# Optimization experiments

Measured on AMD Instinct MI355X. Metric: run time of the kernel, lower is better.

## Reference

```python
import jax, jax.numpy as jnp
import numpy as np

B, N, N_IN, N_OUT, NUM_ACTS = 65536, 512, 64, 16, 5


def setup_inputs() -> dict:
    key = jax.random.key(0)
    k1, k2, k3, k4 = jax.random.split(key, 4)
    input_values = jax.random.normal(k1, (B, N_IN), dtype=jnp.float32)
    # small weights so recurrent pre-activations stay in a sane range
    weight_matrix = jax.random.normal(k2, (N, N), dtype=jnp.float32) * 0.1
    biases = jax.random.normal(k3, (N,), dtype=jnp.float32) * 0.1
    act_ids = jax.random.randint(k4, (N,), 0, NUM_ACTS, dtype=jnp.int32)
    return {
        "input_values": input_values,
        "weight_matrix": weight_matrix,
        "biases": biases,
        "act_ids": act_ids,
    }


def _apply_lut_activations(total, act_ids):
    # Vectorized replacement for the per-neuron Python dispatch loop.
    # act_ids: [N] int, total: [B, N] float. Elementwise select fuses cleanly.
    conds = [act_ids[None, :] == k for k in range(NUM_ACTS)]
    branches = [
        jnp.tanh(total),                      # 0: tanh
        jax.nn.sigmoid(total),                # 1: sigmoid
        jax.nn.relu(total),                   # 2: relu
        jnp.where(total > 0, total, 0.01 * total),  # 3: leaky_relu
        total,                                # 4: identity
    ]
    return jnp.select(conds, branches, total)


def reference(input_values, weight_matrix, biases, act_ids):
    b, n_in = input_values.shape
    n = weight_matrix.shape[0]
    # forward_batch: states start at zeros (refractory multiply on zeros is a no-op),
    # input neurons (first N_IN indices) get the raw input values.
    states = jnp.zeros((b, n), dtype=input_values.dtype).at[:, :n_in].set(input_values)
    total_input = states @ weight_matrix + biases  # [B, N]
    activated = _apply_lut_activations(total_input, act_ids)
    # input-layer neurons keep their raw input values (loop skips layer == 'input')
    is_input = jnp.arange(n) < n_in  # [N]
    new_states = jnp.where(is_input[None, :], states, activated)
    # output neurons are the last N_OUT indices
    return new_states[:, n - N_OUT:]
```

## Files before the change

### kernel.cpp

```cpp
#include <hip/hip_runtime.h>
#include <math.h>


typedef __bf16 bf16x8 __attribute__((ext_vector_type(8)));
typedef float floatx4 __attribute__((ext_vector_type(4)));

#define NN_N 512
#define NN_NIN 64
#define NN_NOUT 16

__global__ __launch_bounds__(256) void NeuralNetwork_74466142978489_kernel(
    const float* __restrict__ x,
    const float* __restrict__ W,
    const float* __restrict__ bias,
    const int*   __restrict__ acts,
    float* __restrict__ out,
    int num_tiles)
{
    const int lane = threadIdx.x & 63;
    const int wave = (int)((blockIdx.x * blockDim.x + threadIdx.x) >> 6);
    const int nwaves = (int)((gridDim.x * blockDim.x) >> 6);
    const int m    = lane & 15;
    const int quad = lane >> 4;
    const int col  = m;
    const int gcol = NN_N - NN_NOUT + col;

    bf16x8 bfrag0, bfrag1;
#pragma unroll
    for (int j = 0; j < 8; ++j) {
        int k0 = quad * 8 + j;
        bfrag0[j] = (__bf16)W[(size_t)k0 * NN_N + gcol];
        bfrag1[j] = (__bf16)W[(size_t)(k0 + 32) * NN_N + gcol];
    }
    const float bval = bias[gcol];
    const int aid = acts[gcol];

    for (int tile = wave; tile < num_tiles; tile += nwaves) {
        const float* row = x + (size_t)(tile * 16 + m) * NN_NIN;

        floatx4 acc = {bval, bval, bval, bval};
#pragma unroll
        for (int t = 0; t < 2; ++t) {
            const float4 a0 = *(const float4*)(row + t * 32 + quad * 8);
            const float4 a1 = *(const float4*)(row + t * 32 + quad * 8 + 4);
            bf16x8 afrag;
            afrag[0] = (__bf16)a0.x; afrag[1] = (__bf16)a0.y;
            afrag[2] = (__bf16)a0.z; afrag[3] = (__bf16)a0.w;
            afrag[4] = (__bf16)a1.x; afrag[5] = (__bf16)a1.y;
            afrag[6] = (__bf16)a1.z; afrag[7] = (__bf16)a1.w;
            acc = __builtin_amdgcn_mfma_f32_16x16x32_bf16(
                afrag, (t == 0) ? bfrag0 : bfrag1, acc, 0, 0, 0);
        }

#pragma unroll
        for (int r = 0; r < 4; ++r) {
            float v = acc[r];
            float y;
            if (aid == 0) {
                y = 1.0f - 2.0f / (__expf(2.0f * v) + 1.0f);
            } else if (aid == 1) {
                y = 1.0f / (1.0f + __expf(-v));
            } else if (aid == 2) {
                y = v > 0.0f ? v : 0.0f;
            } else if (aid == 3) {
                y = v > 0.0f ? v : 0.01f * v;
            } else {
                y = v;
            }
            out[(size_t)(tile * 16 + quad * 4 + r) * NN_NOUT + col] = y;
        }
    }
}

extern "C" void kernel_launch(void* const* d_in, const int* in_sizes, int n_in,
                              void* d_out, int out_size, void* d_ws, size_t ws_size,
                              hipStream_t stream) {
    const float* x    = (const float*)d_in[0];
    const float* W    = (const float*)d_in[1];
    const float* bias = (const float*)d_in[2];
    const int*   acts = (const int*)d_in[3];
    float* out = (float*)d_out;

    const int B = in_sizes[0] / NN_NIN;
    const int num_tiles = B / 16;

    const int block = 256;
    const int waves_per_block = block / 64;
    const int grid = (num_tiles + waves_per_block - 1) / waves_per_block;

    NeuralNetwork_74466142978489_kernel<<<grid, block, 0, stream>>>(
        x, W, bias, acts, out, num_tiles);
}
```

Before: 70.17 us.

## Batch four tiles per wave with nontemporal loads and branchless activations

Each wave now processes groups of four 16-row tiles, issuing all global loads up front with nontemporal hints before running the MFMAs, which puts more memory requests in flight per wave. The activation dispatch becomes branchless: a parameterised sigmoid covers tanh and sigmoid, and fmaxf with a slope covers relu, leaky relu and identity. Output stores are nontemporal and the grid is fixed at 256 blocks with a grid-stride loop instead of one wave per tile. Risks are fewer waves to hide latency, higher register pressure, and dropping any leftover tiles when the tile count is not a multiple of four.

```diff
diff --git a/kernel.cpp b/kernel.cpp
--- a/kernel.cpp
+++ b/kernel.cpp
@@ -8,6 +8,7 @@
 #define NN_N 512
 #define NN_NIN 64
 #define NN_NOUT 16
+#define TPW 4
 
 __global__ __launch_bounds__(256) void NeuralNetwork_74466142978489_kernel(
     const float* __restrict__ x,
@@ -15,15 +16,14 @@
     const float* __restrict__ bias,
     const int*   __restrict__ acts,
     float* __restrict__ out,
-    int num_tiles)
+    int num_groups)
 {
     const int lane = threadIdx.x & 63;
     const int wave = (int)((blockIdx.x * blockDim.x + threadIdx.x) >> 6);
     const int nwaves = (int)((gridDim.x * blockDim.x) >> 6);
     const int m    = lane & 15;
     const int quad = lane >> 4;
-    const int col  = m;
-    const int gcol = NN_N - NN_NOUT + col;
+    const int gcol = NN_N - NN_NOUT + m;
 
     bf16x8 bfrag0, bfrag1;
 #pragma unroll
@@ -35,39 +35,50 @@
     const float bval = bias[gcol];
     const int aid = acts[gcol];
 
-    for (int tile = wave; tile < num_tiles; tile += nwaves) {
-        const float* row = x + (size_t)(tile * 16 + m) * NN_NIN;
+    const bool  is_sig = (aid < 2);
+    const float sA = (aid == 0) ? 2.0f : 1.0f;
+    const float sB = (aid == 0) ? 2.0f : 1.0f;
+    const float sC = (aid == 0) ? -1.0f : 0.0f;
+    const float lc = (aid == 3) ? 0.01f : ((aid == 4) ? 1.0f : 0.0f);
 
-        floatx4 acc = {bval, bval, bval, bval};
+    for (int g = wave; g < num_groups; g += nwaves) {
+        const int tile0 = g * TPW;
+
+        floatx4 a[TPW][4];
 #pragma unroll
-        for (int t = 0; t < 2; ++t) {
-            const float4 a0 = *(const float4*)(row + t * 32 + quad * 8);
-            const float4 a1 = *(const float4*)(row + t * 32 + quad * 8 + 4);
-            bf16x8 afrag;
-            afrag[0] = (__bf16)a0.x; afrag[1] = (__bf16)a0.y;
-            afrag[2] = (__bf16)a0.z; afrag[3] = (__bf16)a0.w;
-            afrag[4] = (__bf16)a1.x; afrag[5] = (__bf16)a1.y;
-            afrag[6] = (__bf16)a1.z; afrag[7] = (__bf16)a1.w;
-            acc = __builtin_amdgcn_mfma_f32_16x16x32_bf16(
-                afrag, (t == 0) ? bfrag0 : bfrag1, acc, 0, 0, 0);
+        for (int t = 0; t < TPW; ++t) {
+            const float* row = x + (size_t)((tile0 + t) * 16 + m) * NN_NIN
+                                 + quad * 8;
+            a[t][0] = __builtin_nontemporal_load((const floatx4*)(row));
+            a[t][1] = __builtin_nontemporal_load((const floatx4*)(row + 4));
+            a[t][2] = __builtin_nontemporal_load((const floatx4*)(row + 32));
+            a[t][3] = __builtin_nontemporal_load((const floatx4*)(row + 36));
         }
 
 #pragma unroll
-        for (int r = 0; r < 4; ++r) {
-            float v = acc[r];
-            float y;
-            if (aid == 0) {
-                y = 1.0f - 2.0f / (__expf(2.0f * v) + 1.0f);
-            } else if (aid == 1) {
-                y = 1.0f / (1.0f + __expf(-v));
-            } else if (aid == 2) {
-                y = v > 0.0f ? v : 0.0f;
-            } else if (aid == 3) {
-                y = v > 0.0f ? v : 0.01f * v;
-            } else {
-                y = v;
+        for (int t = 0; t < TPW; ++t) {
+            bf16x8 af0, af1;
+#pragma unroll
+            for (int j = 0; j < 4; ++j) {
+                af0[j]     = (__bf16)a[t][0][j];
+                af0[4 + j] = (__bf16)a[t][1][j];
+                af1[j]     = (__bf16)a[t][2][j];
+                af1[4 + j] = (__bf16)a[t][3][j];
             }
-            out[(size_t)(tile * 16 + quad * 4 + r) * NN_NOUT + col] = y;
+            floatx4 acc = {bval, bval, bval, bval};
+            acc = __builtin_amdgcn_mfma_f32_16x16x32_bf16(af0, bfrag0, acc, 0, 0, 0);
+            acc = __builtin_amdgcn_mfma_f32_16x16x32_bf16(af1, bfrag1, acc, 0, 0, 0);
+
+            float* obase = out + (size_t)((tile0 + t) * 16 + quad * 4) * NN_NOUT + m;
+#pragma unroll
+            for (int r = 0; r < 4; ++r) {
+                const float v = acc[r];
+                const float lin = fmaxf(v, lc * v);
+                const float s = 1.0f / (1.0f + __expf(-sB * v));
+                const float sig = fmaf(sA, s, sC);
+                const float y = is_sig ? sig : lin;
+                __builtin_nontemporal_store(y, obase + r * NN_NOUT);
+            }
         }
     }
 }
@@ -83,11 +94,11 @@
 
     const int B = in_sizes[0] / NN_NIN;
     const int num_tiles = B / 16;
+    const int num_groups = num_tiles / TPW;
 
     const int block = 256;
-    const int waves_per_block = block / 64;
-    const int grid = (num_tiles + waves_per_block - 1) / waves_per_block;
+    const int grid = 256;
 
     NeuralNetwork_74466142978489_kernel<<<grid, block, 0, stream>>>(
-        x, W, bias, acts, out, num_tiles);
+        x, W, bias, acts, out, num_groups);
 }
```

Result: slower. 71.83 us (+2.4%).
